# Performance work log

Hardware: AMD Instinct MI355X
Metric: run time of the kernel (lower is better)

The kernel has to match this reference:

```python
import jax, jax.numpy as jnp
import numpy as np

GAMMA = 0.99
LAM = 0.95
EPS = 1e-8


def setup_inputs() -> dict:
    key = jax.random.key(0)
    k1, k2, k3 = jax.random.split(key, 3)
    T, N = 2048, 8192
    rewards = jax.random.normal(k1, (T, N), dtype=jnp.float32)
    values = jax.random.normal(k2, (T + 1, N), dtype=jnp.float32)
    dones = jax.random.randint(k3, (T, N), 0, 2, dtype=jnp.int32)
    return {"rewards": rewards, "values": values, "dones": dones}


def reference(rewards, values, dones):
    # rewards: [T, N], values: [T+1, N], dones: [T, N]
    nonterminal = 1.0 - dones.astype(rewards.dtype)        # [T, N]
    # delta_t = r_t + gamma * V_{t+1} * nt_t - V_t
    delta = rewards + GAMMA * values[1:] * nonterminal - values[:-1]
    coef = (GAMMA * LAM) * nonterminal                      # [T, N]

    def step(carry, xs):
        d, c = xs
        a = d + c * carry
        return a, a

    init = jnp.zeros(rewards.shape[1], dtype=rewards.dtype)
    _, advantages = jax.lax.scan(step, init, (delta, coef), reverse=True)
    returns = advantages + values[:-1]
    # torch .std() is unbiased (ddof=1)
    mean = advantages.mean()
    std = advantages.std(ddof=1)
    advantages_norm = (advantages - mean) / (std + EPS)
    return advantages_norm, returns
```

## Files before the change

### kernel.cpp

```cpp
#include <hip/hip_runtime.h>
#include <math.h>

#define GAMMA_ 0.99f
#define GL_ (0.99f * 0.95f)
#define L_ 32

typedef float    f2 __attribute__((ext_vector_type(2)));
typedef int      i2 __attribute__((ext_vector_type(2)));
typedef unsigned u2 __attribute__((ext_vector_type(2)));

__global__ __launch_bounds__(256)
void gae_pass1(const f2* __restrict__ rw, const f2* __restrict__ vv,
               const i2* __restrict__ dn,
               f2* __restrict__ A, f2* __restrict__ B,
               f2* __restrict__ Sa, f2* __restrict__ Sa2,
               f2* __restrict__ SaP, f2* __restrict__ SP,
               f2* __restrict__ SP2, u2* __restrict__ mask,
               int T, int N2)
{
    int q = blockIdx.x * blockDim.x + threadIdx.x;
    int chunk = blockIdx.y;
    if (q >= N2) return;
    int s = chunk * L_;
    int e = s + L_; if (e > T) e = T;

    float a[2]  = {0.f,0.f}, P[2]   = {1.f,1.f};
    float sa[2] = {0.f,0.f}, sa2[2] = {0.f,0.f};
    float saP[2]= {0.f,0.f}, sP[2]  = {0.f,0.f}, sP2[2] = {0.f,0.f};
    unsigned mm[2] = {0u,0u};

    f2 vn = vv[(size_t)e * N2 + q];
    float vnext[2] = {vn.x, vn.y};

    #pragma unroll 4
    for (int t = e - 1; t >= s; --t) {
        size_t off = (size_t)t * N2 + q;
        f2 r2 = rw[off];
        i2 d2 = __builtin_nontemporal_load(&dn[off]);
        f2 v2 = vv[off];
        unsigned bit = 1u << (t - s);
        #pragma unroll
        for (int j = 0; j < 2; ++j) {
            float nt = (d2[j] == 0) ? 1.0f : 0.0f;
            float delta = r2[j] + GAMMA_ * vnext[j] * nt - v2[j];
            float c = GL_ * nt;
            a[j] = delta + c * a[j];
            P[j] = c * P[j];
            sa[j]  += a[j];
            sa2[j] += a[j] * a[j];
            saP[j] += a[j] * P[j];
            sP[j]  += P[j];
            sP2[j] += P[j] * P[j];
            mm[j] |= (d2[j] == 0) ? bit : 0u;
            vnext[j] = v2[j];
        }
    }
    size_t idx = (size_t)chunk * N2 + q;
    f2 o;
    o.x = a[0];   o.y = a[1];   A[idx]   = o;
    o.x = P[0];   o.y = P[1];   B[idx]   = o;
    o.x = sa[0];  o.y = sa[1];  Sa[idx]  = o;
    o.x = sa2[0]; o.y = sa2[1]; Sa2[idx] = o;
    o.x = saP[0]; o.y = saP[1]; SaP[idx] = o;
    o.x = sP[0];  o.y = sP[1];  SP[idx]  = o;
    o.x = sP2[0]; o.y = sP2[1]; SP2[idx] = o;
    u2 om; om.x = mm[0]; om.y = mm[1];
    mask[idx] = om;
}

__global__ __launch_bounds__(1024)
void gae_pass2_ws(const float* __restrict__ A, const float* __restrict__ B,
                  const float* __restrict__ Sa, const float* __restrict__ Sa2,
                  const float* __restrict__ SaP, const float* __restrict__ SP,
                  const float* __restrict__ SP2,
                  float* __restrict__ carry, double* __restrict__ sums,
                  int N, int C)
{
    __shared__ double psum[16], psq[16];
    int wid  = threadIdx.x >> 6;
    int lane = threadIdx.x & 63;
    int nwav = blockDim.x >> 6;
    int n = blockIdx.x * nwav + wid;

    float Ah = 0.f, Bh = 1.f;
    float sa = 0.f, sa2 = 0.f, saP = 0.f, sp = 0.f, sp2 = 0.f;
    bool act = (n < N) && (lane < C);
    size_t idx = (size_t)lane * N + n;
    if (act) {
        Ah = A[idx];  Bh = B[idx];
        sa = Sa[idx]; sa2 = Sa2[idx]; saP = SaP[idx];
        sp = SP[idx]; sp2 = SP2[idx];
    }

    #pragma unroll
    for (int d = 1; d < 64; d <<= 1) {
        float Ad = __shfl_down(Ah, d, 64);
        float Bd = __shfl_down(Bh, d, 64);
        if (lane + d < 64) { Ah = fmaf(Bh, Ad, Ah); Bh *= Bd; }
    }
    float e = __shfl_down(Ah, 1, 64);
    if (lane == 63) e = 0.f;

    double lsum = 0.0, lsq = 0.0;
    if (act) {
        carry[idx] = e;
        lsum = (double)(sa + sp * e);
        lsq  = (double)(sa2 + 2.0f * e * saP + (e * e) * sp2);
    }
    for (int off = 32; off > 0; off >>= 1) {
        lsum += __shfl_down(lsum, off, 64);
        lsq  += __shfl_down(lsq, off, 64);
    }
    if (lane == 0) { psum[wid] = lsum; psq[wid] = lsq; }
    __syncthreads();
    if (threadIdx.x == 0) {
        double s = 0.0, s2 = 0.0;
        for (int w = 0; w < nwav; ++w) { s += psum[w]; s2 += psq[w]; }
        atomicAdd(&sums[0], s);
        atomicAdd(&sums[1], s2);
    }
}

__global__ __launch_bounds__(64)
void gae_pass2_seq(const float* __restrict__ A, const float* __restrict__ B,
                   const float* __restrict__ Sa, const float* __restrict__ Sa2,
                   const float* __restrict__ SaP, const float* __restrict__ SP,
                   const float* __restrict__ SP2,
                   float* __restrict__ carry, double* __restrict__ sums,
                   int N, int C)
{
    int n = blockIdx.x * blockDim.x + threadIdx.x;
    double lsum = 0.0, lsq = 0.0;
    if (n < N) {
        float g = 0.f;
        for (int i = C - 1; i >= 0; --i) {
            int idx = i * N + n;
            carry[idx] = g;
            float e = g;
            lsum += (double)(Sa[idx] + SP[idx] * e);
            lsq  += (double)(Sa2[idx] + 2.0f * e * SaP[idx] + (e * e) * SP2[idx]);
            g = A[idx] + B[idx] * g;
        }
    }
    for (int off = 32; off > 0; off >>= 1) {
        lsum += __shfl_down(lsum, off, 64);
        lsq  += __shfl_down(lsq, off, 64);
    }
    if ((threadIdx.x & 63) == 0) {
        atomicAdd(&sums[0], lsum);
        atomicAdd(&sums[1], lsq);
    }
}

__global__ __launch_bounds__(256)
void gae_pass3(const f2* __restrict__ rw, const f2* __restrict__ vv,
               const u2* __restrict__ mask, const f2* __restrict__ carry,
               const double* __restrict__ sums,
               f2* __restrict__ out_adv, f2* __restrict__ out_ret,
               int T, int N2, double Minv, double Mm1inv)
{
    int q = blockIdx.x * blockDim.x + threadIdx.x;
    int chunk = blockIdx.y;
    if (q >= N2) return;
    int s = chunk * L_;
    int e = s + L_; if (e > T) e = T;

    double S = sums[0], S2 = sums[1];
    float mean = (float)(S * Minv);
    double vard = (S2 - S * S * Minv) * Mm1inv;
    float inv = (float)(1.0 / (sqrt(vard) + 1e-8));

    size_t idx = (size_t)chunk * N2 + q;
    f2 c2 = carry[idx];
    u2 m2 = mask[idx];
    float a[2] = {c2.x, c2.y};
    unsigned mm[2] = {m2.x, m2.y};

    f2 vn = vv[(size_t)e * N2 + q];
    float vnext[2] = {vn.x, vn.y};

    #pragma unroll 4
    for (int t = e - 1; t >= s; --t) {
        size_t off = (size_t)t * N2 + q;
        f2 r2 = rw[off];
        f2 v2 = vv[off];
        unsigned bit = 1u << (t - s);
        f2 oa, orr;
        #pragma unroll
        for (int j = 0; j < 2; ++j) {
            float nt = (mm[j] & bit) ? 1.0f : 0.0f;
            float delta = r2[j] + GAMMA_ * vnext[j] * nt - v2[j];
            a[j] = delta + GL_ * nt * a[j];
            oa[j]  = (a[j] - mean) * inv;
            orr[j] = a[j] + v2[j];
            vnext[j] = v2[j];
        }
        __builtin_nontemporal_store(oa,  &out_adv[off]);
        __builtin_nontemporal_store(orr, &out_ret[off]);
    }
}

extern "C" void kernel_launch(void* const* d_in, const int* in_sizes, int n_in,
                              void* d_out, int out_size, void* d_ws, size_t ws_size,
                              hipStream_t stream)
{
    const float* rw = (const float*)d_in[0];
    const float* vv = (const float*)d_in[1];
    const int*   dn = (const int*)d_in[2];

    long long TN = in_sizes[0];
    long long VN = in_sizes[1];
    int N = (int)(VN - TN);
    int T = (int)(TN / N);
    int N2 = N / 2;
    int C = (T + L_ - 1) / L_;

    char* ws = (char*)d_ws;
    double* sums = (double*)ws;
    size_t cn = (size_t)C * N;
    unsigned* mask = (unsigned*)(ws + 16);
    float* f   = (float*)(ws + 16 + cn * 4);
    float* A   = f;
    float* B   = f + cn;
    float* Sa  = f + 2 * cn;
    float* Sa2 = f + 3 * cn;
    float* SaP = f + 4 * cn;
    float* SP  = f + 5 * cn;
    float* SP2 = f + 6 * cn;
    float* cry = f + 7 * cn;

    hipMemsetAsync(d_ws, 0, 16, stream);

    dim3 blk(256);
    dim3 g1((N2 + 255) / 256, C);
    gae_pass1<<<g1, blk, 0, stream>>>(
        (const f2*)rw, (const f2*)vv, (const i2*)dn,
        (f2*)A, (f2*)B, (f2*)Sa, (f2*)Sa2, (f2*)SaP,
        (f2*)SP, (f2*)SP2, (u2*)mask, T, N2);

    if (C <= 64) {
        int wpb = 16;
        gae_pass2_ws<<<dim3((N + wpb - 1) / wpb), dim3(wpb * 64), 0, stream>>>(
            A, B, Sa, Sa2, SaP, SP, SP2, cry, sums, N, C);
    } else {
        gae_pass2_seq<<<dim3((N + 63) / 64), dim3(64), 0, stream>>>(
            A, B, Sa, Sa2, SaP, SP, SP2, cry, sums, N, C);
    }

    double M = (double)TN;
    gae_pass3<<<g1, blk, 0, stream>>>(
        (const f2*)rw, (const f2*)vv, (const u2*)mask,
        (const f2*)cry, sums,
        (f2*)d_out, (f2*)((float*)d_out + TN),
        T, N2, 1.0 / M, 1.0 / (M - 1.0));
}
```

Before: 318.4 us.

## Switch to scalar per-column threads with fully unrolled preloaded chunk loads

Pass 1 and pass 3 now give each thread one column instead of a float2 pair. For full 32-step chunks they issue all loads into register arrays up front before running the backward recurrence, which exposes many independent memory requests per thread. The separate memset of the reduction sums is removed, and pass 1 zeroes them from one thread instead. This trades wider vector accesses for more memory-level parallelism per thread, at the cost of higher register pressure and possibly lower occupancy.

New measurement: 314.7 us. Within noise of the previous version (-1.2%).

```diff
diff --git a/kernel.cpp b/kernel.cpp
--- a/kernel.cpp
+++ b/kernel.cpp
@@ -5,67 +5,88 @@
 #define GL_ (0.99f * 0.95f)
 #define L_ 32
 
-typedef float    f2 __attribute__((ext_vector_type(2)));
-typedef int      i2 __attribute__((ext_vector_type(2)));
-typedef unsigned u2 __attribute__((ext_vector_type(2)));
-
 __global__ __launch_bounds__(256)
-void gae_pass1(const f2* __restrict__ rw, const f2* __restrict__ vv,
-               const i2* __restrict__ dn,
-               f2* __restrict__ A, f2* __restrict__ B,
-               f2* __restrict__ Sa, f2* __restrict__ Sa2,
-               f2* __restrict__ SaP, f2* __restrict__ SP,
-               f2* __restrict__ SP2, u2* __restrict__ mask,
-               int T, int N2)
-{
-    int q = blockIdx.x * blockDim.x + threadIdx.x;
+void gae_pass1(const float* __restrict__ rw, const float* __restrict__ vv,
+               const int* __restrict__ dn,
+               float* __restrict__ A, float* __restrict__ B,
+               float* __restrict__ Sa, float* __restrict__ Sa2,
+               float* __restrict__ SaP, float* __restrict__ SP,
+               float* __restrict__ SP2, unsigned* __restrict__ mask,
+               double* __restrict__ sums,
+               int T, int N)
+{
+    if (blockIdx.x == 0 && blockIdx.y == 0 && threadIdx.x == 0) {
+        sums[0] = 0.0; sums[1] = 0.0;
+    }
+    int n = blockIdx.x * blockDim.x + threadIdx.x;
     int chunk = blockIdx.y;
-    if (q >= N2) return;
+    if (n >= N) return;
     int s = chunk * L_;
     int e = s + L_; if (e > T) e = T;
-
-    float a[2]  = {0.f,0.f}, P[2]   = {1.f,1.f};
-    float sa[2] = {0.f,0.f}, sa2[2] = {0.f,0.f};
-    float saP[2]= {0.f,0.f}, sP[2]  = {0.f,0.f}, sP2[2] = {0.f,0.f};
-    unsigned mm[2] = {0u,0u};
-
-    f2 vn = vv[(size_t)e * N2 + q];
-    float vnext[2] = {vn.x, vn.y};
-
-    #pragma unroll 4
-    for (int t = e - 1; t >= s; --t) {
-        size_t off = (size_t)t * N2 + q;
-        f2 r2 = rw[off];
-        i2 d2 = __builtin_nontemporal_load(&dn[off]);
-        f2 v2 = vv[off];
-        unsigned bit = 1u << (t - s);
-        #pragma unroll
-        for (int j = 0; j < 2; ++j) {
-            float nt = (d2[j] == 0) ? 1.0f : 0.0f;
-            float delta = r2[j] + GAMMA_ * vnext[j] * nt - v2[j];
+    int len = e - s;
+
+    float a = 0.f, P = 1.f;
+    float sa = 0.f, sa2 = 0.f, saP = 0.f, sP = 0.f, sP2 = 0.f;
+    unsigned mm = 0u;
+
+    if (len == L_) {
+        float r[L_], v[L_ + 1];
+        int   d[L_];
+        #pragma unroll
+        for (int k = 0; k < L_; ++k)
+            r[k] = rw[(size_t)(s + k) * N + n];
+        #pragma unroll
+        for (int k = 0; k <= L_; ++k)
+            v[k] = vv[(size_t)(s + k) * N + n];
+        #pragma unroll
+        for (int k = 0; k < L_; ++k)
+            d[k] = __builtin_nontemporal_load(&dn[(size_t)(s + k) * N + n]);
+
+        #pragma unroll
+        for (int k = L_ - 1; k >= 0; --k) {
+            float nt = (d[k] == 0) ? 1.0f : 0.0f;
+            float delta = r[k] + GAMMA_ * v[k + 1] * nt - v[k];
             float c = GL_ * nt;
-            a[j] = delta + c * a[j];
-            P[j] = c * P[j];
-            sa[j]  += a[j];
-            sa2[j] += a[j] * a[j];
-            saP[j] += a[j] * P[j];
-            sP[j]  += P[j];
-            sP2[j] += P[j] * P[j];
-            mm[j] |= (d2[j] == 0) ? bit : 0u;
-            vnext[j] = v2[j];
-        }
-    }
-    size_t idx = (size_t)chunk * N2 + q;
-    f2 o;
-    o.x = a[0];   o.y = a[1];   A[idx]   = o;
-    o.x = P[0];   o.y = P[1];   B[idx]   = o;
-    o.x = sa[0];  o.y = sa[1];  Sa[idx]  = o;
-    o.x = sa2[0]; o.y = sa2[1]; Sa2[idx] = o;
-    o.x = saP[0]; o.y = saP[1]; SaP[idx] = o;
-    o.x = sP[0];  o.y = sP[1];  SP[idx]  = o;
-    o.x = sP2[0]; o.y = sP2[1]; SP2[idx] = o;
-    u2 om; om.x = mm[0]; om.y = mm[1];
-    mask[idx] = om;
+            a = delta + c * a;
+            P = c * P;
+            sa  += a;
+            sa2 += a * a;
+            saP += a * P;
+            sP  += P;
+            sP2 += P * P;
+            mm |= (d[k] == 0) ? (1u << k) : 0u;
+        }
+    } else {
+        float vnext = vv[(size_t)e * N + n];
+        for (int t = e - 1; t >= s; --t) {
+            size_t off = (size_t)t * N + n;
+            float r = rw[off];
+            int   dd = dn[off];
+            float vc = vv[off];
+            float nt = (dd == 0) ? 1.0f : 0.0f;
+            float delta = r + GAMMA_ * vnext * nt - vc;
+            float c = GL_ * nt;
+            a = delta + c * a;
+            P = c * P;
+            sa  += a;
+            sa2 += a * a;
+            saP += a * P;
+            sP  += P;
+            sP2 += P * P;
+            mm |= (dd == 0) ? (1u << (t - s)) : 0u;
+            vnext = vc;
+        }
+    }
+
+    size_t idx = (size_t)chunk * N + n;
+    A[idx]   = a;
+    B[idx]   = P;
+    Sa[idx]  = sa;
+    Sa2[idx] = sa2;
+    SaP[idx] = saP;
+    SP[idx]  = sP;
+    SP2[idx] = sP2;
+    mask[idx] = mm;
 }
 
 __global__ __launch_bounds__(1024)
@@ -153,50 +174,59 @@
 }
 
 __global__ __launch_bounds__(256)
-void gae_pass3(const f2* __restrict__ rw, const f2* __restrict__ vv,
-               const u2* __restrict__ mask, const f2* __restrict__ carry,
+void gae_pass3(const float* __restrict__ rw, const float* __restrict__ vv,
+               const unsigned* __restrict__ mask, const float* __restrict__ carry,
                const double* __restrict__ sums,
-               f2* __restrict__ out_adv, f2* __restrict__ out_ret,
-               int T, int N2, double Minv, double Mm1inv)
-{
-    int q = blockIdx.x * blockDim.x + threadIdx.x;
+               float* __restrict__ out_adv, float* __restrict__ out_ret,
+               int T, int N, double Minv, double Mm1inv)
+{
+    int n = blockIdx.x * blockDim.x + threadIdx.x;
     int chunk = blockIdx.y;
-    if (q >= N2) return;
+    if (n >= N) return;
     int s = chunk * L_;
     int e = s + L_; if (e > T) e = T;
+    int len = e - s;
 
     double S = sums[0], S2 = sums[1];
     float mean = (float)(S * Minv);
     double vard = (S2 - S * S * Minv) * Mm1inv;
     float inv = (float)(1.0 / (sqrt(vard) + 1e-8));
 
-    size_t idx = (size_t)chunk * N2 + q;
-    f2 c2 = carry[idx];
-    u2 m2 = mask[idx];
-    float a[2] = {c2.x, c2.y};
-    unsigned mm[2] = {m2.x, m2.y};
-
-    f2 vn = vv[(size_t)e * N2 + q];
-    float vnext[2] = {vn.x, vn.y};
-
-    #pragma unroll 4
-    for (int t = e - 1; t >= s; --t) {
-        size_t off = (size_t)t * N2 + q;
-        f2 r2 = rw[off];
-        f2 v2 = vv[off];
-        unsigned bit = 1u << (t - s);
-        f2 oa, orr;
-        #pragma unroll
-        for (int j = 0; j < 2; ++j) {
-            float nt = (mm[j] & bit) ? 1.0f : 0.0f;
-            float delta = r2[j] + GAMMA_ * vnext[j] * nt - v2[j];
-            a[j] = delta + GL_ * nt * a[j];
-            oa[j]  = (a[j] - mean) * inv;
-            orr[j] = a[j] + v2[j];
-            vnext[j] = v2[j];
-        }
-        __builtin_nontemporal_store(oa,  &out_adv[off]);
-        __builtin_nontemporal_store(orr, &out_ret[off]);
+    size_t idx = (size_t)chunk * N + n;
+    float a = carry[idx];
+    unsigned mm = mask[idx];
+
+    if (len == L_) {
+        float r[L_], v[L_ + 1];
+        #pragma unroll
+        for (int k = 0; k < L_; ++k)
+            r[k] = rw[(size_t)(s + k) * N + n];
+        #pragma unroll
+        for (int k = 0; k <= L_; ++k)
+            v[k] = vv[(size_t)(s + k) * N + n];
+
+        #pragma unroll
+        for (int k = L_ - 1; k >= 0; --k) {
+            float nt = (mm & (1u << k)) ? 1.0f : 0.0f;
+            float delta = r[k] + GAMMA_ * v[k + 1] * nt - v[k];
+            a = delta + GL_ * nt * a;
+            size_t off = (size_t)(s + k) * N + n;
+            __builtin_nontemporal_store((a - mean) * inv, &out_adv[off]);
+            __builtin_nontemporal_store(a + v[k],        &out_ret[off]);
+        }
+    } else {
+        float vnext = vv[(size_t)e * N + n];
+        for (int t = e - 1; t >= s; --t) {
+            size_t off = (size_t)t * N + n;
+            float r = rw[off];
+            float vc = vv[off];
+            float nt = (mm & (1u << (t - s))) ? 1.0f : 0.0f;
+            float delta = r + GAMMA_ * vnext * nt - vc;
+            a = delta + GL_ * nt * a;
+            __builtin_nontemporal_store((a - mean) * inv, &out_adv[off]);
+            __builtin_nontemporal_store(a + vc,          &out_ret[off]);
+            vnext = vc;
+        }
     }
 }
 
@@ -212,7 +242,6 @@
     long long VN = in_sizes[1];
     int N = (int)(VN - TN);
     int T = (int)(TN / N);
-    int N2 = N / 2;
     int C = (T + L_ - 1) / L_;
 
     char* ws = (char*)d_ws;
@@ -229,14 +258,10 @@
     float* SP2 = f + 6 * cn;
     float* cry = f + 7 * cn;
 
-    hipMemsetAsync(d_ws, 0, 16, stream);
-
     dim3 blk(256);
-    dim3 g1((N2 + 255) / 256, C);
+    dim3 g1((N + 255) / 256, C);
     gae_pass1<<<g1, blk, 0, stream>>>(
-        (const f2*)rw, (const f2*)vv, (const i2*)dn,
-        (f2*)A, (f2*)B, (f2*)Sa, (f2*)Sa2, (f2*)SaP,
-        (f2*)SP, (f2*)SP2, (u2*)mask, T, N2);
+        rw, vv, dn, A, B, Sa, Sa2, SaP, SP, SP2, mask, sums, T, N);
 
     if (C <= 64) {
         int wpb = 16;
@@ -249,8 +274,7 @@
 
     double M = (double)TN;
     gae_pass3<<<g1, blk, 0, stream>>>(
-        (const f2*)rw, (const f2*)vv, (const u2*)mask,
-        (const f2*)cry, sums,
-        (f2*)d_out, (f2*)((float*)d_out + TN),
-        T, N2, 1.0 / M, 1.0 / (M - 1.0));
-}
+        rw, vv, mask, cry, sums,
+        (float*)d_out, (float*)d_out + TN,
+        T, N, 1.0 / M, 1.0 / (M - 1.0));
+}
```
